# Kernel optimization log

Measured on AMD Instinct MI355X. Metric: run time of the kernel, lower is better.

The kernel has to match this reference:

```python
import jax, jax.numpy as jnp
import numpy as np

B, M, D = 2048, 40, 64          # batch, num fields, embedding dim
HIDDEN = [128, 128, 128]        # CIN layer sizes


def setup_inputs() -> dict:
    key = jax.random.key(0)
    kx, k0, k1, k2 = jax.random.split(key, 4)
    x = jax.random.normal(kx, (B, M, D), dtype=jnp.float32)
    # torch.rand -> uniform [0, 1)
    W0 = jax.random.uniform(k0, (M, M, HIDDEN[0]), dtype=jnp.float32)
    W1 = jax.random.uniform(k1, (M, HIDDEN[0], HIDDEN[1]), dtype=jnp.float32)
    W2 = jax.random.uniform(k2, (M, HIDDEN[1], HIDDEN[2]), dtype=jnp.float32)
    return {"x": x, "W0": W0, "W1": W1, "W2": W2}


def _cin_forward(x, Ws):
    # x: [b, m, d]. Each layer k:
    #   x_next[b, l, d] = sum_{m, h} x0[b, m, d] * x_k[b, h, d] * W_k[m, h, l]
    # which equals the torch 'bil,bjl->bjil' outer product followed by
    # 'bijk,ijl->bkl' + transpose, but expressed as one fused contraction
    # (opt_einsum picks a path avoiding the worst intermediate).
    ps = []
    xk = x  # [b, H_k, d], H_0 = m
    for W in Ws:
        x_next = jnp.einsum('bmd,bhd,mhl->bld', x, xk, W)  # [b, L_k, d]
        ps.append(jnp.sum(x_next, axis=2))                  # [b, L_k]
        xk = x_next
    return jnp.concatenate(ps, axis=1)                      # [b, sum(L_k)]


def reference(x, W0, W1, W2):
    return _cin_forward(x, (W0, W1, W2))
```

## Files before the change

kernel.cpp:

```cpp
#include <hip/hip_runtime.h>
#include <hip/hip_bf16.h>
#include <cstdint>

#define BATCH 2048
#define MF    40
#define DDIM  64
#define LDIM  128
#define ROWS  (BATCH * DDIM)

typedef __attribute__((ext_vector_type(4)))  short   short4_t;
typedef __attribute__((ext_vector_type(8)))  short   short8;
typedef __attribute__((ext_vector_type(8)))  __bf16  bf16x8;
typedef __attribute__((ext_vector_type(4)))  float   floatx4;
typedef __attribute__((ext_vector_type(16))) float   floatx16;

__device__ __forceinline__ unsigned short f32_to_bf16(float f) {
    union { float f; uint32_t u; } v; v.f = f;
    uint32_t u = v.u;
    uint32_t r = (u + 0x7fffu + ((u >> 16) & 1u)) >> 16;
    return (unsigned short)r;
}

__global__ void k_wprep(const float* __restrict__ W, unsigned short* __restrict__ Wt,
                        int KK, int H) {
    int bi = blockIdx.x;
    int lane = threadIdx.x;
    int cb = bi & 3;
    int mkk = bi >> 2;
    int kk = mkk % KK, m = mkk / KK;
    int l = cb * 32 + (lane & 31);
    int hbase = kk * 16 + (lane >> 5) * 8;
    unsigned short o[8];
#pragma unroll
    for (int j = 0; j < 8; ++j) {
        int h = hbase + j;
        float v = (h < H) ? W[((size_t)m * H + h) * LDIM + l] : 0.f;
        o[j] = f32_to_bf16(v);
    }
    *(short8*)(Wt + ((size_t)bi * 64 + lane) * 8) = *(const short8*)o;
}

template <int KK, bool FIRST, int OFF, bool WRITEX>
__global__ __launch_bounds__(256, 2) void k_gemm(
    const float* __restrict__ x,
    const unsigned short* __restrict__ Xprev,
    const unsigned short* __restrict__ Wt,
    unsigned short* __restrict__ Xout,
    float* __restrict__ out)
{
    __shared__ unsigned short slab[2][KK * 2048];

    const int tid  = threadIdx.x;
    const int lane = tid & 63, wave = tid >> 6;
    const int hf   = lane >> 5, r31 = lane & 31;
    const int rowhalf = wave >> 1, colhalf = wave & 1;
    const int b = blockIdx.x * 2 + rowhalf;

    bf16x8 afrag[2][KK];
    if constexpr (FIRST) {
#pragma unroll
        for (int t = 0; t < 2; ++t)
#pragma unroll
            for (int kk = 0; kk < KK; ++kk) {
                unsigned short tmp[8];
#pragma unroll
                for (int j = 0; j < 8; ++j) {
                    int h = kk * 16 + hf * 8 + j;
                    float v = (h < MF) ? x[((size_t)b * MF + h) * DDIM + t * 32 + r31] : 0.f;
                    tmp[j] = f32_to_bf16(v);
                }
                afrag[t][kk] = __builtin_bit_cast(bf16x8, *(const short8*)tmp);
            }
    } else {
        const int g = r31 >> 3, hs = (r31 >> 2) & 1, ii = r31 & 3;
#pragma unroll
        for (int t = 0; t < 2; ++t) {
            int tile = b * 2 + t;
#pragma unroll
            for (int kk = 0; kk < KK; ++kk) {
                int k0  = kk * 16 + hf * 8;
                int cbk = k0 >> 5, rr = k0 & 31;
                const unsigned short* p =
                    Xprev + ((size_t)(((tile * 4 + cbk) * 4 + g) * 2 + hs) * 32 + rr) * 4 + ii;
                unsigned short tmp[8];
#pragma unroll
                for (int j = 0; j < 8; ++j) tmp[j] = p[(size_t)j * 4];
                afrag[t][kk] = __builtin_bit_cast(bf16x8, *(const short8*)tmp);
            }
        }
    }

    floatx16 acc[2][2] = {};

    auto stage = [&](int m, int buf) {
        const unsigned short* src = Wt + (size_t)m * (KK * 2048);
#pragma unroll
        for (int it = 0; it < KK; ++it) {
            int c = it * 256 + tid;
            __builtin_amdgcn_global_load_lds(
                (const __attribute__((address_space(1))) uint32_t*)(src + (size_t)c * 8),
                (__attribute__((address_space(3))) uint32_t*)(&slab[buf][(size_t)c * 8]),
                16, 0, 0);
        }
    };

    const int cbg0 = colhalf * 2, cbg1 = colhalf * 2 + 1;
    auto ldfrag = [&](const unsigned short* sl, int kk, int cb) {
        return __builtin_bit_cast(
            bf16x8, *(const short8*)(sl + ((size_t)(kk * 4 + cb) * 64 + lane) * 8));
    };

    constexpr int D = (KK < 3) ? KK : 3;

    stage(0, 0);
#pragma unroll 1
    for (int m = 0; m < MF; ++m) {
        asm volatile("s_waitcnt vmcnt(0)" ::: "memory");
        __syncthreads();

        const floatx4* sp4 = (const floatx4*)(x + ((size_t)b * MF + m) * DDIM);
        floatx4 sc0[4], sc1[4];
#pragma unroll
        for (int g = 0; g < 4; ++g) {
            sc0[g] = sp4[hf + 2 * g];
            sc1[g] = sp4[8 + hf + 2 * g];
        }
        if (m + 1 < MF) stage(m + 1, (m + 1) & 1);

        const unsigned short* sl = slab[m & 1];

        bf16x8 bbuf[D][2];
#pragma unroll
        for (int p = 0; p < D; ++p) {
            bbuf[p][0] = ldfrag(sl, p, cbg0);
            bbuf[p][1] = ldfrag(sl, p, cbg1);
        }

        floatx16 P[2][2] = {};
#pragma unroll
        for (int kk = 0; kk < KK; ++kk) {
            const int slot = kk % D;
            P[0][0] = __builtin_amdgcn_mfma_f32_32x32x16_bf16(afrag[0][kk], bbuf[slot][0], P[0][0], 0, 0, 0);
            P[1][0] = __builtin_amdgcn_mfma_f32_32x32x16_bf16(afrag[1][kk], bbuf[slot][0], P[1][0], 0, 0, 0);
            P[0][1] = __builtin_amdgcn_mfma_f32_32x32x16_bf16(afrag[0][kk], bbuf[slot][1], P[0][1], 0, 0, 0);
            P[1][1] = __builtin_amdgcn_mfma_f32_32x32x16_bf16(afrag[1][kk], bbuf[slot][1], P[1][1], 0, 0, 0);
            if (kk + D < KK) {
                bbuf[slot][0] = ldfrag(sl, kk + D, cbg0);
                bbuf[slot][1] = ldfrag(sl, kk + D, cbg1);
            }
        }

#pragma unroll
        for (int cbp = 0; cbp < 2; ++cbp)
#pragma unroll
            for (int g = 0; g < 4; ++g)
#pragma unroll
                for (int i = 0; i < 4; ++i) {
                    acc[0][cbp][g * 4 + i] += sc0[g][i] * P[0][cbp][g * 4 + i];
                    acc[1][cbp][g * 4 + i] += sc1[g][i] * P[1][cbp][g * 4 + i];
                }
    }

    if constexpr (WRITEX) {
#pragma unroll
        for (int t = 0; t < 2; ++t) {
            int tile = b * 2 + t;
#pragma unroll
            for (int cbp = 0; cbp < 2; ++cbp) {
                int cb = colhalf * 2 + cbp;
#pragma unroll
                for (int g = 0; g < 4; ++g) {
                    unsigned short o[4];
#pragma unroll
                    for (int i = 0; i < 4; ++i) o[i] = f32_to_bf16(acc[t][cbp][g * 4 + i]);
                    *(short4_t*)(Xout +
                        ((size_t)(((tile * 4 + cb) * 4 + g) * 2 + hf) * 32 + r31) * 4) =
                        *(const short4_t*)o;
                }
            }
        }
    }

#pragma unroll
    for (int cbp = 0; cbp < 2; ++cbp) {
        float v = 0.f;
#pragma unroll
        for (int j = 0; j < 16; ++j) v += acc[0][cbp][j] + acc[1][cbp][j];
        v += __shfl_xor(v, 32);
        if (hf == 0)
            out[(size_t)b * 384 + OFF + (colhalf * 2 + cbp) * 32 + r31] = v;
    }
}

extern "C" void kernel_launch(void* const* d_in, const int* in_sizes, int n_in,
                              void* d_out, int out_size, void* d_ws, size_t ws_size,
                              hipStream_t stream) {
    const float* x  = (const float*)d_in[0];
    const float* W0 = (const float*)d_in[1];
    const float* W1 = (const float*)d_in[2];
    const float* W2 = (const float*)d_in[3];
    float* out = (float*)d_out;

    char* ws = (char*)d_ws;
    size_t off = 0;
    auto alloc = [&](size_t bytes) -> void* {
        void* p = ws + off;
        off += (bytes + 255) & ~(size_t)255;
        return p;
    };
    unsigned short* W0t = (unsigned short*)alloc((size_t)MF * 3 * 2048 * 2);
    unsigned short* W1t = (unsigned short*)alloc((size_t)MF * 8 * 2048 * 2);
    unsigned short* W2t = (unsigned short*)alloc((size_t)MF * 8 * 2048 * 2);
    unsigned short* X1p = (unsigned short*)alloc((size_t)ROWS * LDIM * 2);
    unsigned short* X2p = (unsigned short*)alloc((size_t)ROWS * LDIM * 2);

    k_wprep<<<MF * 3 * 4, 64, 0, stream>>>(W0, W0t, 3, 40);
    k_wprep<<<MF * 8 * 4, 64, 0, stream>>>(W1, W1t, 8, 128);
    k_wprep<<<MF * 8 * 4, 64, 0, stream>>>(W2, W2t, 8, 128);

    k_gemm<3, true,  0,   true ><<<ROWS / 128, 256, 0, stream>>>(x, nullptr, W0t, X1p, out);
    k_gemm<8, false, 128, true ><<<ROWS / 128, 256, 0, stream>>>(x, X1p,     W1t, X2p, out);
    k_gemm<8, false, 256, false><<<ROWS / 128, 256, 0, stream>>>(x, X2p,     W2t, X2p, out);
}
```

Measured before the change: 465.8 us.

## Pipeline weight staging across m with a 4-slot LDS ring and partial waits

Replaces the per-m double-buffered weight slab, which waited for all loads and synchronised once per m, with a 4-deep ring of sub-chunks of KU k-steps. Loads run three chunks ahead and use partial vmcnt waits with raw barriers. B fragments are prefetched across m boundaries, so the MFMA stream no longer stalls at the start of each m. The aim is to hide global-to-LDS latency and cut barrier stalls. The cost is hand-tuned vmcnt counts, which are fragile: a wrong count or a reordered scalar load could cause a race.

```diff
diff --git a/kernel.cpp b/kernel.cpp
--- a/kernel.cpp
+++ b/kernel.cpp
@@ -8,17 +8,28 @@
 #define LDIM  128
 #define ROWS  (BATCH * DDIM)
 
-typedef __attribute__((ext_vector_type(4)))  short   short4_t;
-typedef __attribute__((ext_vector_type(8)))  short   short8;
-typedef __attribute__((ext_vector_type(8)))  __bf16  bf16x8;
-typedef __attribute__((ext_vector_type(4)))  float   floatx4;
-typedef __attribute__((ext_vector_type(16))) float   floatx16;
+typedef __attribute__((ext_vector_type(4)))  short    short4_t;
+typedef __attribute__((ext_vector_type(8)))  short    short8;
+typedef __attribute__((ext_vector_type(8)))  __bf16   bf16x8;
+typedef __attribute__((ext_vector_type(4)))  float    floatx4;
+typedef __attribute__((ext_vector_type(16))) float    floatx16;
 
 __device__ __forceinline__ unsigned short f32_to_bf16(float f) {
     union { float f; uint32_t u; } v; v.f = f;
     uint32_t u = v.u;
     uint32_t r = (u + 0x7fffu + ((u >> 16) & 1u)) >> 16;
     return (unsigned short)r;
+}
+
+__device__ __forceinline__ void barrier_raw() {
+    asm volatile("s_barrier" ::: "memory");
+}
+template <int N> __device__ __forceinline__ void vmwait() {
+    if constexpr (N == 0)  asm volatile("s_waitcnt vmcnt(0)"  ::: "memory");
+    if constexpr (N == 3)  asm volatile("s_waitcnt vmcnt(3)"  ::: "memory");
+    if constexpr (N == 4)  asm volatile("s_waitcnt vmcnt(4)"  ::: "memory");
+    if constexpr (N == 11) asm volatile("s_waitcnt vmcnt(11)" ::: "memory");
+    if constexpr (N == 12) asm volatile("s_waitcnt vmcnt(12)" ::: "memory");
 }
 
 __global__ void k_wprep(const float* __restrict__ W, unsigned short* __restrict__ Wt,
@@ -40,7 +51,7 @@
     *(short8*)(Wt + ((size_t)bi * 64 + lane) * 8) = *(const short8*)o;
 }
 
-template <int KK, bool FIRST, int OFF, bool WRITEX>
+template <int KK, int KU, bool FIRST, int OFF, bool WRITEX>
 __global__ __launch_bounds__(256, 2) void k_gemm(
     const float* __restrict__ x,
     const unsigned short* __restrict__ Xprev,
@@ -48,7 +59,12 @@
     unsigned short* __restrict__ Xout,
     float* __restrict__ out)
 {
-    __shared__ unsigned short slab[2][KK * 2048];
+    constexpr int UPM   = KK / KU;
+    constexpr int NU    = MF * UPM;
+    constexpr int DIST  = (KU == 4) ? 2 : 3;
+    constexpr int SLOTS = (KU == 4) ? 2 : 3;
+
+    __shared__ unsigned short slab[4][KU * 2048];
 
     const int tid  = threadIdx.x;
     const int lane = tid & 63, wave = tid >> 6;
@@ -92,64 +108,76 @@
 
     floatx16 acc[2][2] = {};
 
-    auto stage = [&](int m, int buf) {
-        const unsigned short* src = Wt + (size_t)m * (KK * 2048);
-#pragma unroll
-        for (int it = 0; it < KK; ++it) {
+    auto stage = [&](int uu) {
+        int u = uu < NU ? uu : NU - 1;
+        const unsigned short* src = Wt + (size_t)u * (KU * 2048);
+#pragma unroll
+        for (int it = 0; it < KU; ++it) {
             int c = it * 256 + tid;
             __builtin_amdgcn_global_load_lds(
                 (const __attribute__((address_space(1))) uint32_t*)(src + (size_t)c * 8),
-                (__attribute__((address_space(3))) uint32_t*)(&slab[buf][(size_t)c * 8]),
+                (__attribute__((address_space(3))) uint32_t*)(&slab[u & 3][(size_t)c * 8]),
                 16, 0, 0);
         }
     };
 
     const int cbg0 = colhalf * 2, cbg1 = colhalf * 2 + 1;
-    auto ldfrag = [&](const unsigned short* sl, int kk, int cb) {
-        return __builtin_bit_cast(
-            bf16x8, *(const short8*)(sl + ((size_t)(kk * 4 + cb) * 64 + lane) * 8));
+    auto ldfrag = [&](int u, int frag, int cb) {
+        return __builtin_bit_cast(bf16x8,
+            *(const short8*)(&slab[u & 3][((size_t)(frag * 4 + cb) * 64 + lane) * 8]));
     };
 
-    constexpr int D = (KK < 3) ? KK : 3;
-
-    stage(0, 0);
+    vmwait<0>();
+    stage(0); stage(1); stage(2);
+    vmwait<(KU == 4) ? 4 : 3>();
+    barrier_raw();
+
+    bf16x8 bbuf[SLOTS][2];
+#pragma unroll
+    for (int p = 0; p < SLOTS; ++p) {
+        bbuf[p][0] = ldfrag(0, p, cbg0);
+        bbuf[p][1] = ldfrag(0, p, cbg1);
+    }
+
+    floatx4 sc0[4], sc1[4];
+
 #pragma unroll 1
     for (int m = 0; m < MF; ++m) {
-        asm volatile("s_waitcnt vmcnt(0)" ::: "memory");
-        __syncthreads();
-
-        const floatx4* sp4 = (const floatx4*)(x + ((size_t)b * MF + m) * DDIM);
-        floatx4 sc0[4], sc1[4];
-#pragma unroll
-        for (int g = 0; g < 4; ++g) {
-            sc0[g] = sp4[hf + 2 * g];
-            sc1[g] = sp4[8 + hf + 2 * g];
-        }
-        if (m + 1 < MF) stage(m + 1, (m + 1) & 1);
-
-        const unsigned short* sl = slab[m & 1];
-
-        bf16x8 bbuf[D][2];
-#pragma unroll
-        for (int p = 0; p < D; ++p) {
-            bbuf[p][0] = ldfrag(sl, p, cbg0);
-            bbuf[p][1] = ldfrag(sl, p, cbg1);
-        }
-
         floatx16 P[2][2] = {};
 #pragma unroll
         for (int kk = 0; kk < KK; ++kk) {
-            const int slot = kk % D;
+            if (kk % KU == 0) {
+                barrier_raw();
+                if (kk == 0) {
+                    const floatx4* sp4 = (const floatx4*)(x + ((size_t)b * MF + m) * DDIM);
+#pragma unroll
+                    for (int g = 0; g < 4; ++g) {
+                        sc0[g] = sp4[hf + 2 * g];
+                        sc1[g] = sp4[8 + hf + 2 * g];
+                    }
+                }
+                stage(m * UPM + kk / KU + 3);
+            }
+            const int slot = (KU == 4) ? (kk & 1) : kk;
             P[0][0] = __builtin_amdgcn_mfma_f32_32x32x16_bf16(afrag[0][kk], bbuf[slot][0], P[0][0], 0, 0, 0);
             P[1][0] = __builtin_amdgcn_mfma_f32_32x32x16_bf16(afrag[1][kk], bbuf[slot][0], P[1][0], 0, 0, 0);
             P[0][1] = __builtin_amdgcn_mfma_f32_32x32x16_bf16(afrag[0][kk], bbuf[slot][1], P[0][1], 0, 0, 0);
             P[1][1] = __builtin_amdgcn_mfma_f32_32x32x16_bf16(afrag[1][kk], bbuf[slot][1], P[1][1], 0, 0, 0);
-            if (kk + D < KK) {
-                bbuf[slot][0] = ldfrag(sl, kk + D, cbg0);
-                bbuf[slot][1] = ldfrag(sl, kk + D, cbg1);
-            }
-        }
-
+            {
+                const int j  = kk + DIST;
+                int mm = m + ((j >= KK) ? 1 : 0);
+                if (mm > MF - 1) mm = MF - 1;
+                const int jj = (j >= KK) ? (j - KK) : j;
+                const int u  = mm * UPM + jj / KU;
+                bbuf[slot][0] = ldfrag(u, jj % KU, cbg0);
+                bbuf[slot][1] = ldfrag(u, jj % KU, cbg1);
+            }
+            if (kk % KU == KU - 1) {
+                if (KU == 3)      vmwait<11>();
+                else if (kk == 3) vmwait<12>();
+                else              vmwait<4>();
+            }
+        }
 #pragma unroll
         for (int cbp = 0; cbp < 2; ++cbp)
 #pragma unroll
@@ -218,7 +246,7 @@
     k_wprep<<<MF * 8 * 4, 64, 0, stream>>>(W1, W1t, 8, 128);
     k_wprep<<<MF * 8 * 4, 64, 0, stream>>>(W2, W2t, 8, 128);
 
-    k_gemm<3, true,  0,   true ><<<ROWS / 128, 256, 0, stream>>>(x, nullptr, W0t, X1p, out);
-    k_gemm<8, false, 128, true ><<<ROWS / 128, 256, 0, stream>>>(x, X1p,     W1t, X2p, out);
-    k_gemm<8, false, 256, false><<<ROWS / 128, 256, 0, stream>>>(x, X2p,     W2t, X2p, out);
-}
+    k_gemm<3, 3, true,  0,   true ><<<ROWS / 128, 256, 0, stream>>>(x, nullptr, W0t, X1p, out);
+    k_gemm<8, 4, false, 128, true ><<<ROWS / 128, 256, 0, stream>>>(x, X1p,     W1t, X2p, out);
+    k_gemm<8, 4, false, 256, false><<<ROWS / 128, 256, 0, stream>>>(x, X2p,     W2t, X2p, out);
+}
```

Result: no change. 460.0 us (-1.2%).
